# Kernel tuning notes

Hardware: AMD Instinct MI355X
Metric: run time of the kernel (lower is better)

Reference implementation:

```python
import jax, jax.numpy as jnp
import numpy as np

B, T, C = 2, 2048, 2048
H, KVH = 16, 4
HD = C // H            # head_dim = 128
REP = H // KVH         # q heads per kv head = 4


def _alibi_slopes(n_head):
    # get_slopes_power_of_2: start = 2^(-2^-(log2(H)-3)); s_h = start * start^h
    start = 2.0 ** (-(2.0 ** (-(np.log2(n_head) - 3.0))))
    return jnp.asarray([start ** (i + 1) for i in range(n_head)], jnp.float32)


def setup_inputs() -> dict:
    key = jax.random.key(0)
    ks = jax.random.split(key, 4)
    sc = 0.02
    return {
        "x": jax.random.normal(ks[0], (B, T, C), jnp.float32),
        "Wq": jax.random.normal(ks[1], (C, C), jnp.float32) * sc,
        "Wkv": jax.random.normal(ks[2], (C, HD * KVH * 2), jnp.float32) * sc,
        "Wo": jax.random.normal(ks[3], (C, C), jnp.float32) * sc,
        "bo": jnp.zeros((C,), jnp.float32),
    }


def reference(x, Wq, Wkv, Wo, bo):
    Bv, Tv, Cv = x.shape
    # projections
    q = (x @ Wq).reshape(Bv, Tv, H, HD).transpose(0, 2, 1, 3)      # (B,H,T,hd)
    k, v = jnp.split(x @ Wkv, 2, axis=-1)
    k = k.reshape(Bv, Tv, KVH, HD).transpose(0, 2, 1, 3)           # (B,KVH,T,hd)
    v = v.reshape(Bv, Tv, KVH, HD).transpose(0, 2, 1, 3)
    # torch .repeat tiles kv heads: query head h = r*KVH + g uses kv head g.
    qg = q.reshape(Bv, REP, KVH, Tv, HD)
    scores = jnp.einsum('brgtd,bgsd->brgts', qg, k) / jnp.sqrt(jnp.float32(HD))
    # ALiBi bias: tril((j - i) * slope_h), zero on/above diagonal region handled by causal mask
    idx = jnp.arange(Tv)
    diff = (idx[None, :] - idx[:, None]).astype(jnp.float32)       # j - i (negative below diag)
    slopes = _alibi_slopes(H).reshape(REP, KVH)                    # head h = r*KVH+g
    bias = jnp.tril(diff)[None, None] * slopes[:, :, None, None]   # (REP,KVH,T,T)
    causal = idx[None, :] <= idx[:, None]                          # (T,T)
    scores = jnp.where(causal[None, None, None], scores + bias[None], -jnp.inf)
    attn = jax.nn.softmax(scores, axis=-1)
    out = jnp.einsum('brgts,bgsd->brgtd', attn, v)                 # (B,REP,KVH,T,hd)
    out = out.reshape(Bv, H, Tv, HD).transpose(0, 2, 1, 3).reshape(Bv, Tv, Cv)
    return out @ Wo + bo
```

## Files before the change

### kernel.cpp

```cpp
#include <hip/hip_runtime.h>

typedef __attribute__((ext_vector_type(8))) __bf16 bf16x8;
typedef __attribute__((ext_vector_type(4))) float f32x4;

#define NEG_BIG (-1e30f)

__device__ __forceinline__ unsigned short f2b(float f) {
    unsigned int u = __float_as_uint(f);
    u += 0x7FFFu + ((u >> 16) & 1u);
    return (unsigned short)(u >> 16);
}
__device__ __forceinline__ float b2f(unsigned short h) {
    return __uint_as_float(((unsigned int)h) << 16);
}
__device__ __forceinline__ unsigned cvtpk(float lo, float hi) {
    unsigned r;
    asm("v_cvt_pk_bf16_f32 %0, %1, %2" : "=v"(r) : "v"(lo), "v"(hi));
    return r;
}

typedef const __attribute__((address_space(1))) unsigned int* gas_ptr;
typedef __attribute__((address_space(3))) unsigned int* las_ptr;
__device__ __forceinline__ void gload16(const void* g, void* l) {
    __builtin_amdgcn_global_load_lds((gas_ptr)g, (las_ptr)l, 16, 0, 0);
}

__global__ __launch_bounds__(256) void k_convert(
    const float* __restrict__ x, unsigned short* __restrict__ xb, int n4)
{
    int i = blockIdx.x * 256 + threadIdx.x;
    if (i >= n4) return;
    float4 v = reinterpret_cast<const float4*>(x)[i];
    ushort4 h;
    h.x = f2b(v.x); h.y = f2b(v.y); h.z = f2b(v.z); h.w = f2b(v.w);
    reinterpret_cast<ushort4*>(xb)[i] = h;
}

__global__ __launch_bounds__(256) void k_transpose(
    const float* __restrict__ W, unsigned short* __restrict__ Th, int K, int N)
{
    __shared__ float tile[64][65];
    const int n0 = blockIdx.x * 64, k0 = blockIdx.y * 64;
    const int c = threadIdx.x & 63, r0 = threadIdx.x >> 6;
    for (int rr = r0; rr < 64; rr += 4)
        tile[rr][c] = W[(size_t)(k0 + rr) * N + n0 + c];
    __syncthreads();
    for (int rr = r0; rr < 64; rr += 4)
        Th[(size_t)(n0 + rr) * K + k0 + c] = f2b(tile[c][rr]);
}

__global__ __launch_bounds__(256) void k_gemm(
    const unsigned short* __restrict__ A, const unsigned short* __restrict__ B,
    void* __restrict__ CoutA, int NA, void* __restrict__ CoutB, int NB, int N1,
    const float* __restrict__ bias, int M, int K, int outF32)
{
    __shared__ __align__(16) unsigned short As[128][32];
    __shared__ __align__(16) unsigned short Bs[128][32];

    const int tid  = threadIdx.x;
    const int lane = tid & 63, wid = tid >> 6;
    const int wr = wid >> 1, wc = wid & 1;
    const int lrow = lane & 15, lko = (lane >> 4) << 3;
    const int trow = tid >> 2, tk = (tid & 3) << 3;
    const int bm = blockIdx.y, bn = blockIdx.x;
    const int wbyte = wid * 1024;

    f32x4 acc[4][4] = {};

    const size_t aoff = (size_t)(bm * 128 + trow) * K + tk;
    const size_t boff = (size_t)(bn * 128 + trow) * K + tk;
    const size_t half = (size_t)64 * K;

    for (int k0 = 0; k0 < K; k0 += 32) {
        gload16(&A[aoff + k0],        (char*)&As[0][0] + wbyte);
        gload16(&A[aoff + half + k0], (char*)&As[0][0] + 4096 + wbyte);
        gload16(&B[boff + k0],        (char*)&Bs[0][0] + wbyte);
        gload16(&B[boff + half + k0], (char*)&Bs[0][0] + 4096 + wbyte);
        __syncthreads();

        bf16x8 af[4], bf[4];
        #pragma unroll
        for (int m = 0; m < 4; ++m)
            af[m] = *reinterpret_cast<const bf16x8*>(&As[wr * 64 + m * 16 + lrow][lko]);
        #pragma unroll
        for (int n = 0; n < 4; ++n)
            bf[n] = *reinterpret_cast<const bf16x8*>(&Bs[wc * 64 + n * 16 + lrow][lko]);
        #pragma unroll
        for (int m = 0; m < 4; ++m)
            #pragma unroll
            for (int n = 0; n < 4; ++n)
                acc[m][n] = __builtin_amdgcn_mfma_f32_16x16x32_bf16(af[m], bf[n], acc[m][n], 0, 0, 0);
        __syncthreads();
    }

    const int rbase = bm * 128 + wr * 64 + ((lane >> 4) << 2);
    const int cbase = bn * 128 + wc * 64 + lrow;
    #pragma unroll
    for (int m = 0; m < 4; ++m)
        #pragma unroll
        for (int n = 0; n < 4; ++n) {
            const int col = cbase + n * 16;
            const float bv = bias ? bias[col] : 0.0f;
            const bool inA = (col < N1);
            const int ccol = inA ? col : (col - N1);
            const int cstr = inA ? NA : NB;
            void* base = inA ? CoutA : CoutB;
            #pragma unroll
            for (int r = 0; r < 4; ++r) {
                const size_t idx = (size_t)(rbase + m * 16 + r) * cstr + ccol;
                const float v = acc[m][n][r] + bv;
                if (outF32) ((float*)base)[idx] = v;
                else        ((unsigned short*)base)[idx] = f2b(v);
            }
        }
}

__global__ __launch_bounds__(512, 4) void k_attn(
    const unsigned short* __restrict__ Qb,
    const unsigned short* __restrict__ KVb,
    unsigned short* __restrict__ AO)
{
    __shared__ __align__(16) unsigned short Ksl[64][128];
    __shared__ __align__(16) unsigned short Vt[128][72];
    __shared__ __align__(16) unsigned short Psl[8][16][72];

    const int blk = blockIdx.x;
    const int ord = blk >> 3;
    const int sub = blk & 7;
    const int b   = sub >> 2;
    const int g   = sub & 3;
    const int q0  = (63 - ord) * 32;

    const int tid = threadIdx.x;
    const int lane = tid & 63;
    const int w = tid >> 6;
    const int h = (w & 3) * 4 + g;
    const int q0w = q0 + (w >> 2) * 16;
    const float slope = exp2f(-0.5f * (float)(h + 1));
    const float isq = 0.088388347648318447f;
    const int lrow = lane & 15;
    const int lko  = (lane >> 4) << 3;
    const int rowg = (lane >> 4) << 2;
    const int skey = tid >> 4;
    const int sd0  = (tid & 15) << 3;
    const int vdim = tid & 127;
    const int vkg  = tid >> 7;

    uint4 kreg[2];
    unsigned short vv[2][8];

    auto ldK = [&](int kb) {
        const int j0 = kb << 6;
        #pragma unroll
        for (int pp = 0; pp < 2; ++pp) {
            const int key = skey + pp * 32;
            kreg[pp] = *reinterpret_cast<const uint4*>(
                &KVb[(size_t)(b * 2048 + j0 + key) * 1024 + g * 128 + sd0]);
        }
    };
    auto wrK = [&]() {
        #pragma unroll
        for (int pp = 0; pp < 2; ++pp) {
            const int key = skey + pp * 32;
            *reinterpret_cast<uint4*>(&Ksl[key][sd0 ^ ((key & 7) << 3)]) = kreg[pp];
        }
    };
    auto ldV = [&](int kb) {
        const int j0 = kb << 6;
        #pragma unroll
        for (int gi = 0; gi < 2; ++gi) {
            const int kgi = gi * 4 + vkg;
            const size_t base = (size_t)(b * 2048 + j0 + kgi * 8) * 1024 + 512 + g * 128 + vdim;
            #pragma unroll
            for (int j = 0; j < 8; ++j)
                vv[gi][j] = KVb[base + (size_t)j * 1024];
        }
    };
    auto wrV = [&]() {
        #pragma unroll
        for (int gi = 0; gi < 2; ++gi) {
            const int kgi = gi * 4 + vkg;
            *reinterpret_cast<uint4*>(&Vt[vdim][kgi * 8]) =
                *reinterpret_cast<const uint4*>(&vv[gi][0]);
        }
    };

    bf16x8 qf[4];
    {
        const size_t qoff = (size_t)(b * 2048 + q0w + lrow) * 2048 + h * 128 + lko;
        #pragma unroll
        for (int kk = 0; kk < 4; ++kk)
            qf[kk] = *reinterpret_cast<const bf16x8*>(&Qb[qoff + kk * 32]);
    }

    f32x4 oacc[8] = {};
    float mrow = NEG_BIG, lsum = 0.f;
    const int nkb = (q0 + 32 + 63) >> 6;
    const int q = q0w + lrow;

    ldK(0); ldV(0);
    wrK(); wrV();
    __syncthreads();

    for (int kb = 0; kb < nkb; ++kb) {
        const int j0 = kb << 6;
        const bool pre = (kb + 1 < nkb);
        if (pre) { ldK(kb + 1); ldV(kb + 1); }

        f32x4 sa[4] = {};
        #pragma unroll
        for (int c = 0; c < 4; ++c) {
            const int krow = c * 16 + lrow;
            #pragma unroll
            for (int kk = 0; kk < 4; ++kk) {
                bf16x8 kf = *reinterpret_cast<const bf16x8*>(
                    &Ksl[krow][(kk * 32 + lko) ^ ((krow & 7) << 3)]);
                sa[c] = __builtin_amdgcn_mfma_f32_16x16x32_bf16(kf, qf[kk], sa[c], 0, 0, 0);
            }
        }

        float pv[4][4];
        float mt = NEG_BIG;
        #pragma unroll
        for (int c = 0; c < 4; ++c)
            #pragma unroll
            for (int r = 0; r < 4; ++r) {
                const int j = j0 + c * 16 + rowg + r;
                const float vsc = (j <= q) ? (sa[c][r] * isq + slope * (float)(j - q)) : NEG_BIG;
                pv[c][r] = vsc;
                mt = fmaxf(mt, vsc);
            }
        mt = fmaxf(mt, __shfl_xor(mt, 16));
        mt = fmaxf(mt, __shfl_xor(mt, 32));
        const float mn = fmaxf(mrow, mt);
        const float alpha = __expf(mrow - mn);
        mrow = mn;
        float s = 0.f;
        #pragma unroll
        for (int c = 0; c < 4; ++c)
            #pragma unroll
            for (int r = 0; r < 4; ++r) {
                const float pe = __expf(pv[c][r] - mn);
                pv[c][r] = pe;
                s += pe;
            }
        s += __shfl_xor(s, 16);
        s += __shfl_xor(s, 32);
        lsum = lsum * alpha + s;

        float ar[4];
        #pragma unroll
        for (int r = 0; r < 4; ++r) ar[r] = __shfl(alpha, rowg + r);
        #pragma unroll
        for (int f = 0; f < 8; ++f)
            #pragma unroll
            for (int r = 0; r < 4; ++r)
                oacc[f][r] *= ar[r];

        #pragma unroll
        for (int c = 0; c < 4; ++c) {
            uint2 pw;
            pw.x = cvtpk(pv[c][0], pv[c][1]);
            pw.y = cvtpk(pv[c][2], pv[c][3]);
            *reinterpret_cast<uint2*>(&Psl[w][lrow][c * 16 + rowg]) = pw;
        }
        asm volatile("s_waitcnt lgkmcnt(0)" ::: "memory");

        #pragma unroll
        for (int kk2 = 0; kk2 < 2; ++kk2) {
            bf16x8 pf = *reinterpret_cast<const bf16x8*>(&Psl[w][lrow][kk2 * 32 + lko]);
            #pragma unroll
            for (int nb = 0; nb < 8; ++nb) {
                bf16x8 vf = *reinterpret_cast<const bf16x8*>(&Vt[nb * 16 + lrow][kk2 * 32 + lko]);
                oacc[nb] = __builtin_amdgcn_mfma_f32_16x16x32_bf16(pf, vf, oacc[nb], 0, 0, 0);
            }
        }

        __syncthreads();
        if (pre) { wrK(); wrV(); }
        __syncthreads();
    }

    float lr[4];
    #pragma unroll
    for (int r = 0; r < 4; ++r) lr[r] = __shfl(lsum, rowg + r);
    #pragma unroll
    for (int nb = 0; nb < 8; ++nb)
        #pragma unroll
        for (int r = 0; r < 4; ++r) {
            const int row = q0w + rowg + r;
            const int col = h * 128 + nb * 16 + lrow;
            const float vo = oacc[nb][r] / lr[r];
            AO[(size_t)(b * 2048 + row) * 2048 + col] = f2b(vo);
        }
}

extern "C" void kernel_launch(void* const* d_in, const int* in_sizes, int n_in,
                              void* d_out, int out_size, void* d_ws, size_t ws_size,
                              hipStream_t stream)
{
    const float* x   = (const float*)d_in[0];
    const float* Wq  = (const float*)d_in[1];
    const float* Wkv = (const float*)d_in[2];
    const float* Wo  = (const float*)d_in[3];
    const float* bo  = (const float*)d_in[4];

    char* ws = (char*)d_ws;
    unsigned short* xb  = (unsigned short*)(ws + (size_t)0);
    unsigned short* Wt  = (unsigned short*)(ws + ((size_t)16 << 20));
    unsigned short* Qb  = (unsigned short*)(ws + ((size_t)28 << 20));
    unsigned short* KVb = (unsigned short*)(ws + ((size_t)44 << 20));

    k_convert<<<8192, 256, 0, stream>>>(x, xb, (2 * 2048 * 2048) / 4);

    k_transpose<<<dim3(32, 32), 256, 0, stream>>>(Wq, Wt, 2048, 2048);
    k_transpose<<<dim3(16, 32), 256, 0, stream>>>(Wkv, Wt + (size_t)2048 * 2048, 2048, 1024);

    k_gemm<<<dim3(24, 32), 256, 0, stream>>>(xb, Wt, Qb, 2048, KVb, 1024, 2048,
                                             nullptr, 4096, 2048, 0);

    k_attn<<<512, 512, 0, stream>>>(Qb, KVb, xb);

    k_transpose<<<dim3(32, 32), 256, 0, stream>>>(Wo, Wt, 2048, 2048);
    k_gemm<<<dim3(16, 32), 256, 0, stream>>>(xb, Wt, d_out, 2048, nullptr, 2048, 2048,
                                             bo, 4096, 2048, 1);
}
```

Before: 268.5 us.

## Load K fragments directly from global and double-buffer V in LDS

K tiles are no longer staged through shared memory. Each wave reads its MFMA K fragments straight from global memory, relying on L1/L2 reuse across the eight waves. V is now double-buffered in LDS, which removes one of the two block barriers per key block. The cost is redundant global K traffic, since every wave re-reads the same K rows, and the K loads sit on the critical path before the QK MFMAs.

```diff
diff --git a/kernel.cpp b/kernel.cpp
--- a/kernel.cpp
+++ b/kernel.cpp
@@ -120,8 +120,7 @@
     const unsigned short* __restrict__ KVb,
     unsigned short* __restrict__ AO)
 {
-    __shared__ __align__(16) unsigned short Ksl[64][128];
-    __shared__ __align__(16) unsigned short Vt[128][72];
+    __shared__ __align__(16) unsigned short Vt[2][128][72];
     __shared__ __align__(16) unsigned short Psl[8][16][72];
 
     const int blk = blockIdx.x;
@@ -141,30 +140,11 @@
     const int lrow = lane & 15;
     const int lko  = (lane >> 4) << 3;
     const int rowg = (lane >> 4) << 2;
-    const int skey = tid >> 4;
-    const int sd0  = (tid & 15) << 3;
     const int vdim = tid & 127;
     const int vkg  = tid >> 7;
 
-    uint4 kreg[2];
     unsigned short vv[2][8];
 
-    auto ldK = [&](int kb) {
-        const int j0 = kb << 6;
-        #pragma unroll
-        for (int pp = 0; pp < 2; ++pp) {
-            const int key = skey + pp * 32;
-            kreg[pp] = *reinterpret_cast<const uint4*>(
-                &KVb[(size_t)(b * 2048 + j0 + key) * 1024 + g * 128 + sd0]);
-        }
-    };
-    auto wrK = [&]() {
-        #pragma unroll
-        for (int pp = 0; pp < 2; ++pp) {
-            const int key = skey + pp * 32;
-            *reinterpret_cast<uint4*>(&Ksl[key][sd0 ^ ((key & 7) << 3)]) = kreg[pp];
-        }
-    };
     auto ldV = [&](int kb) {
         const int j0 = kb << 6;
         #pragma unroll
@@ -176,11 +156,11 @@
                 vv[gi][j] = KVb[base + (size_t)j * 1024];
         }
     };
-    auto wrV = [&]() {
+    auto wrV = [&](int buf) {
         #pragma unroll
         for (int gi = 0; gi < 2; ++gi) {
             const int kgi = gi * 4 + vkg;
-            *reinterpret_cast<uint4*>(&Vt[vdim][kgi * 8]) =
+            *reinterpret_cast<uint4*>(&Vt[buf][vdim][kgi * 8]) =
                 *reinterpret_cast<const uint4*>(&vv[gi][0]);
         }
     };
@@ -197,24 +177,25 @@
     float mrow = NEG_BIG, lsum = 0.f;
     const int nkb = (q0 + 32 + 63) >> 6;
     const int q = q0w + lrow;
-
-    ldK(0); ldV(0);
-    wrK(); wrV();
+    const size_t kbase = (size_t)(b * 2048 + lrow) * 1024 + g * 128 + lko;
+
+    ldV(0);
+    wrV(0);
     __syncthreads();
 
+    int cur = 0;
     for (int kb = 0; kb < nkb; ++kb) {
         const int j0 = kb << 6;
         const bool pre = (kb + 1 < nkb);
-        if (pre) { ldK(kb + 1); ldV(kb + 1); }
+        if (pre) ldV(kb + 1);
 
         f32x4 sa[4] = {};
         #pragma unroll
         for (int c = 0; c < 4; ++c) {
-            const int krow = c * 16 + lrow;
+            const size_t rb = kbase + (size_t)(j0 + c * 16) * 1024;
             #pragma unroll
             for (int kk = 0; kk < 4; ++kk) {
-                bf16x8 kf = *reinterpret_cast<const bf16x8*>(
-                    &Ksl[krow][(kk * 32 + lko) ^ ((krow & 7) << 3)]);
+                bf16x8 kf = *reinterpret_cast<const bf16x8*>(&KVb[rb + kk * 32]);
                 sa[c] = __builtin_amdgcn_mfma_f32_16x16x32_bf16(kf, qf[kk], sa[c], 0, 0, 0);
             }
         }
@@ -271,14 +252,14 @@
             bf16x8 pf = *reinterpret_cast<const bf16x8*>(&Psl[w][lrow][kk2 * 32 + lko]);
             #pragma unroll
             for (int nb = 0; nb < 8; ++nb) {
-                bf16x8 vf = *reinterpret_cast<const bf16x8*>(&Vt[nb * 16 + lrow][kk2 * 32 + lko]);
+                bf16x8 vf = *reinterpret_cast<const bf16x8*>(&Vt[cur][nb * 16 + lrow][kk2 * 32 + lko]);
                 oacc[nb] = __builtin_amdgcn_mfma_f32_16x16x32_bf16(pf, vf, oacc[nb], 0, 0, 0);
             }
         }
 
+        if (pre) wrV(cur ^ 1);
         __syncthreads();
-        if (pre) { wrK(); wrV(); }
-        __syncthreads();
+        cur ^= 1;
     }
 
     float lr[4];
```

After: 374.4 us. 39.5% more time.
